# Kernel optimization log

Measured on AMD Instinct MI355X. Metric: run time of the kernel, lower is better.

Reference implementation:

```python
import jax, jax.numpy as jnp
import numpy as np

N_NODES = 50000
N_EDGES = 500000
IN_DIM = 128
H1, C1 = 4, 64   # layer1: heads=4, out=64, concat -> 256
H2, C2 = 1, 64   # layer2: heads=1, out=64


def setup_inputs() -> dict:
    key = jax.random.key(0)
    ks = jax.random.split(key, 16)
    p = lambda k, shp: (jax.random.normal(k, shp, dtype=jnp.float32) * 0.1)
    return {
        "x": jax.random.normal(ks[0], (N_NODES, IN_DIM), dtype=jnp.float32),
        "edge_index": jax.random.randint(ks[1], (2, N_EDGES), 0, N_NODES, dtype=jnp.int32),
        "edge_attr": jax.random.uniform(ks[2], (N_EDGES, 1), dtype=jnp.float32),
        # layer 1 params
        "W1": p(ks[3], (IN_DIM, H1 * C1)),
        "We1": p(ks[4], (1, H1 * C1)),
        "as1": p(ks[5], (H1, C1)),
        "ad1": p(ks[6], (H1, C1)),
        "ae1": p(ks[7], (H1, C1)),
        "b1": jnp.zeros((H1 * C1,), dtype=jnp.float32),
        # layer 2 params
        "W2": p(ks[8], (H1 * C1, H2 * C2)),
        "We2": p(ks[9], (1, H2 * C2)),
        "as2": p(ks[10], (H2, C2)),
        "ad2": p(ks[11], (H2, C2)),
        "ae2": p(ks[12], (H2, C2)),
        "b2": jnp.zeros((H2 * C2,), dtype=jnp.float32),
    }


def _add_self_loops(src, dst, edge_attr, n):
    # PyG fill_value='mean': loop edge_attr = mean of incoming edge attrs per node
    cnt = jax.ops.segment_sum(jnp.ones((src.shape[0],), edge_attr.dtype), dst, num_segments=n)
    loop_attr = jax.ops.segment_sum(edge_attr, dst, num_segments=n) / jnp.maximum(cnt, 1.0)[:, None]
    idx = jnp.arange(n, dtype=src.dtype)
    return (jnp.concatenate([src, idx]), jnp.concatenate([dst, idx]),
            jnp.concatenate([edge_attr, loop_attr], axis=0))


def _gat_conv(x, src, dst, edge_attr, W, We, a_src, a_dst, a_edge, bias, heads, out_ch):
    n = x.shape[0]
    h = (x @ W).reshape(n, heads, out_ch)                      # [N,H,C]
    e = (edge_attr @ We).reshape(-1, heads, out_ch)            # [E,H,C]
    alpha = ((h * a_src).sum(-1)[src]                          # gather src score
             + (h * a_dst).sum(-1)[dst]                        # gather dst score
             + (e * a_edge).sum(-1))                           # [E,H]
    alpha = jax.nn.leaky_relu(alpha, 0.2)
    m = jax.ops.segment_max(alpha, dst, num_segments=n)        # per-target max
    alpha = jnp.exp(alpha - m[dst])
    denom = jax.ops.segment_sum(alpha, dst, num_segments=n)
    alpha = alpha / (denom[dst] + 1e-16)
    out = jax.ops.segment_sum(h[src] * alpha[..., None], dst, num_segments=n)
    return out.reshape(n, heads * out_ch) + bias


def reference(x, edge_index, edge_attr, W1, We1, as1, ad1, ae1, b1,
              W2, We2, as2, ad2, ae2, b2):
    src, dst = edge_index[0], edge_index[1]
    src, dst, ea = _add_self_loops(src, dst, edge_attr, x.shape[0])
    h = jax.nn.elu(_gat_conv(x, src, dst, ea, W1, We1, as1, ad1, ae1, b1, H1, C1))
    return _gat_conv(h, src, dst, ea, W2, We2, as2, ad2, ae2, b2, H2, C2)
```

## Files before the change

### kernel.cpp

```cpp
#include <hip/hip_runtime.h>
#include <math.h>

#define NN 50000
#define NE 500000
#define DIM 128
#define HC1 256
#define HC2 64
#define RSTR 64
#define CAPM 63
#define EPB 1024
#define NBUCKET ((NE + EPB - 1) / EPB)
#define GB ((NN + 63) / 64)

typedef __attribute__((ext_vector_type(8))) short short8;
typedef __attribute__((ext_vector_type(4))) float floatx4;


__device__ __forceinline__ unsigned short f2bf(float f) {
  unsigned int u = __float_as_uint(f);
  unsigned int r = (u + 0x7FFFu + ((u >> 16) & 1u)) >> 16;
  return (unsigned short)r;
}
__device__ __forceinline__ float bf2f(unsigned short s) {
  return __uint_as_float(((unsigned int)s) << 16);
}

__device__ __forceinline__ float waveReduce(float v) {
  v += __shfl_down(v, 32);
  v += __shfl_down(v, 16);
  v += __shfl_down(v, 8);
  v += __shfl_down(v, 4);
  v += __shfl_down(v, 2);
  v += __shfl_down(v, 1);
  return v;
}


__global__ __launch_bounds__(256) void k_prep(const float* __restrict__ W1,
                                              const float* __restrict__ W2,
                                              const float* __restrict__ We1,
                                              const float* __restrict__ ae1,
                                              const float* __restrict__ We2,
                                              const float* __restrict__ ae2,
                                              unsigned short* __restrict__ W1T,
                                              unsigned short* __restrict__ W2T,
                                              float* __restrict__ ce,
                                              unsigned int* __restrict__ ebuf) {
  int b = blockIdx.x, t = threadIdx.x;
  if (b < 128) {
    int idx = b * 256 + t;
    int n = idx >> 7, k = idx & 127;
    W1T[idx] = f2bf(W1[k * 256 + n]);
  } else if (b < 192) {
    int idx = (b - 128) * 256 + t;
    int n = idx >> 8, k = idx & 255;
    W2T[idx] = f2bf(W2[k * 64 + n]);
  } else if (b == 192) {
    int h = t >> 6, lane = t & 63;
    float p = We1[h * 64 + lane] * ae1[h * 64 + lane];
    p = waveReduce(p);
    if (lane == 0) ce[h] = p;
    if (h == 0) {
      float q = We2[lane] * ae2[lane];
      q = waveReduce(q);
      if (lane == 0) ce[4] = q;
    }
  } else {
    int idx = (b - 193) * 256 + t;
    if (idx < NN) ebuf[(unsigned long long)idx * RSTR] = 0u;
  }
}


__global__ __launch_bounds__(256) void k_fused(const int* __restrict__ src,
                                               const int* __restrict__ dst,
                                               const float* __restrict__ ea,
                                               unsigned int* __restrict__ ebuf,
                                               const float* __restrict__ x,
                                               const unsigned short* __restrict__ W1T,
                                               const float* __restrict__ as1,
                                               const float* __restrict__ ad1,
                                               unsigned short* __restrict__ h1b,
                                               float* __restrict__ ss1,
                                               float* __restrict__ sd1) {
  __shared__ unsigned short As[64 * 136];
  int t = threadIdx.x;

  if (blockIdx.x < NBUCKET) {
    int e0 = blockIdx.x * EPB + t;
    int dv[4]; float ev[4]; unsigned int sv[4]; bool ok[4];
#pragma unroll
    for (int k = 0; k < 4; k++) {
      int e = e0 + k * 256;
      ok[k] = (e < NE);
      int ee = ok[k] ? e : 0;
      dv[k] = dst[ee];
      ev[k] = ea[ee];
      sv[k] = (unsigned int)src[ee];
    }
    unsigned int old[4];
#pragma unroll
    for (int k = 0; k < 4; k++) {
      if (ok[k]) old[k] = atomicAdd(&ebuf[(unsigned long long)dv[k] * RSTR], 1u);
    }
#pragma unroll
    for (int k = 0; k < 4; k++) {
      if (ok[k] && old[k] < CAPM) {
        unsigned int ea16 = __float2uint_rn(ev[k] * 65536.0f);
        if (ea16 > 65535u) ea16 = 65535u;
        ebuf[(unsigned long long)dv[k] * RSTR + 1 + old[k]] = (ea16 << 16) | sv[k];
      }
    }
    return;
  }

  int wave = t >> 6, lane = t & 63;
  int q = lane >> 4, ln = lane & 15;
  int m0 = (blockIdx.x - NBUCKET) * 64;
  int n0 = wave * 64;

  short8 bfr[4][4];
#pragma unroll
  for (int c = 0; c < 4; c++)
#pragma unroll
    for (int ks = 0; ks < 4; ks++)
      bfr[c][ks] = *(const short8*)&W1T[(n0 + ln * 4 + c) * 128 + ks * 32 + q * 8];

#pragma unroll
  for (int rep = 0; rep < 8; rep++) {
    int chunk = t + 256 * rep;
    int m = chunk >> 5, kk = (chunk & 31) * 4;
    int gr = m0 + m;
    float4 v = (gr < NN) ? *(const float4*)&x[gr * DIM + kk]
                         : make_float4(0.f, 0.f, 0.f, 0.f);
    ushort4 o;
    o.x = f2bf(v.x); o.y = f2bf(v.y); o.z = f2bf(v.z); o.w = f2bf(v.w);
    *(ushort4*)&As[m * 136 + kk] = o;
  }
  __syncthreads();

  floatx4 acc[4][4];
#pragma unroll
  for (int r = 0; r < 4; r++)
#pragma unroll
    for (int c = 0; c < 4; c++) acc[r][c] = (floatx4){0.f, 0.f, 0.f, 0.f};

#pragma unroll
  for (int ks = 0; ks < 4; ks++) {
    short8 afr[4];
#pragma unroll
    for (int r = 0; r < 4; r++)
      afr[r] = *(const short8*)&As[(r * 16 + ln) * 136 + ks * 32 + q * 8];
#pragma unroll
    for (int r = 0; r < 4; r++)
#pragma unroll
      for (int c = 0; c < 4; c++)
        acc[r][c] = __builtin_amdgcn_mfma_f32_16x16x32_bf16(afr[r], bfr[c][ks], acc[r][c], 0, 0, 0);
  }

  float4 a4 = *(const float4*)&as1[n0 + ln * 4];
  float4 d4 = *(const float4*)&ad1[n0 + ln * 4];

#pragma unroll
  for (int r = 0; r < 4; r++) {
#pragma unroll
    for (int i = 0; i < 4; i++) {
      int gm = m0 + r * 16 + q * 4 + i;
      if (gm < NN) {
        ushort4 o;
        o.x = f2bf(acc[r][0][i]);
        o.y = f2bf(acc[r][1][i]);
        o.z = f2bf(acc[r][2][i]);
        o.w = f2bf(acc[r][3][i]);
        *(ushort4*)&h1b[gm * HC1 + n0 + ln * 4] = o;
      }
      float ps = acc[r][0][i] * a4.x;
      float pd = acc[r][0][i] * d4.x;
      ps = fmaf(acc[r][1][i], a4.y, ps);
      pd = fmaf(acc[r][1][i], d4.y, pd);
      ps = fmaf(acc[r][2][i], a4.z, ps);
      pd = fmaf(acc[r][2][i], d4.z, pd);
      ps = fmaf(acc[r][3][i], a4.w, ps);
      pd = fmaf(acc[r][3][i], d4.w, pd);
#pragma unroll
      for (int m = 1; m < 16; m <<= 1) {
        ps += __shfl_xor(ps, m);
        pd += __shfl_xor(pd, m);
      }
      if (ln == 0 && gm < NN) {
        ss1[gm * 4 + wave] = ps;
        sd1[gm * 4 + wave] = pd;
      }
    }
  }
}


__global__ __launch_bounds__(1024) void k_agg1g2(const unsigned short* __restrict__ h1b,
                                                 const unsigned int* __restrict__ ebuf,
                                                 const float* __restrict__ ss1,
                                                 const float* __restrict__ sd1,
                                                 const float* __restrict__ ce,
                                                 const float* __restrict__ b1,
                                                 const unsigned short* __restrict__ W2T,
                                                 const float* __restrict__ as2,
                                                 const float* __restrict__ ad2,
                                                 unsigned short* __restrict__ h2b,
                                                 float* __restrict__ ss2,
                                                 float* __restrict__ sd2) {
  __shared__ unsigned short Ao[64 * 264];
  __shared__ float ssp[4][64], sdp[4][64];
  int t = threadIdx.x;
  int wave = t >> 6, lane = t & 63;
  int m0 = blockIdx.x * 64;

  {
    int h = lane >> 4;
    int c4 = lane * 4;
    int l16 = lane & 15;
    float ceh = ce[h];
    float4 bv = *(const float4*)&b1[c4];

    for (int nd = 0; nd < 4; nd++) {
      int vu = m0 + wave * 4 + nd;
      int lrow = wave * 4 + nd;
      if (vu >= NN) {
        ushort4 z = {0, 0, 0, 0};
        *(ushort4*)&Ao[lrow * 264 + c4] = z;
        continue;
      }
      unsigned int craw = ebuf[(unsigned long long)vu * RSTR];
      int cn = (craw < CAPM) ? (int)craw : CAPM;
      cn = __builtin_amdgcn_readfirstlane(cn);
      int beg1 = vu * RSTR + 1;
      int end1 = beg1 + cn;
      float sdh = sd1[vu * 4 + h];
      float4 acc = make_float4(0.f, 0.f, 0.f, 0.f);
      float l = 0.f;
      float easum = 0.f;

      for (int base = beg1; base < end1; base += 16) {
        unsigned int meta = ebuf[base + l16];
#pragma unroll
        for (int b4 = 0; b4 < 4; b4++) {
          if (base + b4 * 4 >= end1) break;
          float ssv[4], ea4[4];
          ushort4 u[4];
          bool vld[4];
#pragma unroll
          for (int jj = 0; jj < 4; jj++) {
            int j = b4 * 4 + jj;
            bool val = (base + j < end1);
            unsigned int m = __builtin_amdgcn_readlane(meta, j);
            int sj = val ? (int)(m & 0xFFFFu) : 0;
            ea4[jj] = (float)(m >> 16) * (1.0f / 65536.0f);
            vld[jj] = val;
            ssv[jj] = ss1[sj * 4 + h];
            u[jj] = *(const ushort4*)&h1b[sj * HC1 + c4];
          }
#pragma unroll
          for (int jj = 0; jj < 4; jj++) {
            easum += vld[jj] ? ea4[jj] : 0.f;
            float xx = fmaf(ea4[jj], ceh, ssv[jj] + sdh);
            xx = fmaxf(xx, 0.2f * xx);
            float a = vld[jj] ? __expf(xx) : 0.f;
            l += a;
            acc.x = fmaf(a, bf2f(u[jj].x), acc.x);
            acc.y = fmaf(a, bf2f(u[jj].y), acc.y);
            acc.z = fmaf(a, bf2f(u[jj].z), acc.z);
            acc.w = fmaf(a, bf2f(u[jj].w), acc.w);
          }
        }
      }
      {
        float lea = easum / fmaxf((float)cn, 1.0f);
        float xx = fmaf(lea, ceh, ss1[vu * 4 + h] + sdh);
        xx = fmaxf(xx, 0.2f * xx);
        float a = __expf(xx);
        ushort4 u = *(const ushort4*)&h1b[vu * HC1 + c4];
        l += a;
        acc.x = fmaf(a, bf2f(u.x), acc.x);
        acc.y = fmaf(a, bf2f(u.y), acc.y);
        acc.z = fmaf(a, bf2f(u.z), acc.z);
        acc.w = fmaf(a, bf2f(u.w), acc.w);
      }
      float inv = 1.f / (l + 1e-16f);
      float4 o;
      o.x = acc.x * inv + bv.x;
      o.y = acc.y * inv + bv.y;
      o.z = acc.z * inv + bv.z;
      o.w = acc.w * inv + bv.w;
      o.x = (o.x > 0.f) ? o.x : expm1f(o.x);
      o.y = (o.y > 0.f) ? o.y : expm1f(o.y);
      o.z = (o.z > 0.f) ? o.z : expm1f(o.z);
      o.w = (o.w > 0.f) ? o.w : expm1f(o.w);
      ushort4 ob;
      ob.x = f2bf(o.x); ob.y = f2bf(o.y); ob.z = f2bf(o.z); ob.w = f2bf(o.w);
      *(ushort4*)&Ao[lrow * 264 + c4] = ob;
    }
  }
  __syncthreads();

  {
    int q = lane >> 4, ln = lane & 15;
    int r = wave >> 2, c = wave & 3;

    short8 bfr[8];
#pragma unroll
    for (int ks = 0; ks < 8; ks++)
      bfr[ks] = *(const short8*)&W2T[(c * 16 + ln) * 256 + ks * 32 + q * 8];

    floatx4 acc = (floatx4){0.f, 0.f, 0.f, 0.f};
#pragma unroll
    for (int ks = 0; ks < 8; ks++) {
      short8 afr = *(const short8*)&Ao[(r * 16 + ln) * 264 + ks * 32 + q * 8];
      acc = __builtin_amdgcn_mfma_f32_16x16x32_bf16(afr, bfr[ks], acc, 0, 0, 0);
    }

    float as2v = as2[c * 16 + ln], ad2v = ad2[c * 16 + ln];
#pragma unroll
    for (int i = 0; i < 4; i++) {
      int gm = m0 + r * 16 + q * 4 + i;
      if (gm < NN) h2b[gm * HC2 + c * 16 + ln] = f2bf(acc[i]);
      float ps = acc[i] * as2v;
      float pd = acc[i] * ad2v;
#pragma unroll
      for (int m = 1; m < 16; m <<= 1) {
        ps += __shfl_xor(ps, m);
        pd += __shfl_xor(pd, m);
      }
      if (ln == 0) {
        ssp[c][r * 16 + q * 4 + i] = ps;
        sdp[c][r * 16 + q * 4 + i] = pd;
      }
    }
  }
  __syncthreads();
  if (t < 64) {
    int gm = m0 + t;
    if (gm < NN) {
      ss2[gm] = ssp[0][t] + ssp[1][t] + ssp[2][t] + ssp[3][t];
      sd2[gm] = sdp[0][t] + sdp[1][t] + sdp[2][t] + sdp[3][t];
    }
  }
}

__global__ __launch_bounds__(256) void k_agg2(const unsigned short* __restrict__ h2b,
                                              const unsigned int* __restrict__ ebuf,
                                              const float* __restrict__ ss2,
                                              const float* __restrict__ sd2,
                                              const float* __restrict__ ce,
                                              const float* __restrict__ b2,
                                              float* __restrict__ out) {
  int v = (blockIdx.x * blockDim.x + threadIdx.x) >> 6;
  int lane = threadIdx.x & 63;
  int g = lane >> 4;
  int c = lane & 15;
  int l16 = lane & 15;
  int vu = __builtin_amdgcn_readfirstlane(v);
  unsigned int craw = ebuf[(unsigned long long)vu * RSTR];
  int cn = (craw < CAPM) ? (int)craw : CAPM;
  cn = __builtin_amdgcn_readfirstlane(cn);
  int beg1 = vu * RSTR + 1;
  int end1 = beg1 + cn;
  float sdv = sd2[vu];
  float cev = ce[4];
  float4 acc = make_float4(0.f, 0.f, 0.f, 0.f);
  float l = 0.f;
  float easum = 0.f;

  for (int base = beg1; base < end1; base += 16) {
    int nb = end1 - base;
    unsigned int meta = ebuf[base + l16];
    float ssv[4], eav[4];
    bool vld[4];
    ushort4 u[4];
#pragma unroll
    for (int sub = 0; sub < 4; sub++) {
      int j = sub * 4 + g;
      bool val = (j < nb);
      unsigned int m = (unsigned int)__shfl((int)meta, j);
      int sj = val ? (int)(m & 0xFFFFu) : 0;
      eav[sub] = (float)(m >> 16) * (1.0f / 65536.0f);
      vld[sub] = val;
      ssv[sub] = ss2[sj];
      u[sub] = *(const ushort4*)&h2b[sj * HC2 + c * 4];
    }
#pragma unroll
    for (int sub = 0; sub < 4; sub++) {
      easum += vld[sub] ? eav[sub] : 0.f;
      float xx = fmaf(eav[sub], cev, ssv[sub] + sdv);
      xx = fmaxf(xx, 0.2f * xx);
      float a = vld[sub] ? __expf(xx) : 0.f;
      l += a;
      acc.x = fmaf(a, bf2f(u[sub].x), acc.x);
      acc.y = fmaf(a, bf2f(u[sub].y), acc.y);
      acc.z = fmaf(a, bf2f(u[sub].z), acc.z);
      acc.w = fmaf(a, bf2f(u[sub].w), acc.w);
    }
  }
#pragma unroll
  for (int m = 16; m <= 32; m <<= 1) {
    acc.x += __shfl_xor(acc.x, m);
    acc.y += __shfl_xor(acc.y, m);
    acc.z += __shfl_xor(acc.z, m);
    acc.w += __shfl_xor(acc.w, m);
    l += __shfl_xor(l, m);
    easum += __shfl_xor(easum, m);
  }
  {
    float lea = easum / fmaxf((float)cn, 1.0f);
    float xx = fmaf(lea, cev, ss2[vu] + sdv);
    xx = fmaxf(xx, 0.2f * xx);
    float a = __expf(xx);
    ushort4 us = *(const ushort4*)&h2b[vu * HC2 + c * 4];
    l += a;
    acc.x = fmaf(a, bf2f(us.x), acc.x);
    acc.y = fmaf(a, bf2f(us.y), acc.y);
    acc.z = fmaf(a, bf2f(us.z), acc.z);
    acc.w = fmaf(a, bf2f(us.w), acc.w);
  }
  if (g == 0) {
    float inv = 1.f / (l + 1e-16f);
    float4 bv = *(const float4*)&b2[c * 4];
    float4 o;
    o.x = acc.x * inv + bv.x;
    o.y = acc.y * inv + bv.y;
    o.z = acc.z * inv + bv.z;
    o.w = acc.w * inv + bv.w;
    *(float4*)&out[vu * HC2 + c * 4] = o;
  }
}


extern "C" void kernel_launch(void* const* d_in, const int* in_sizes, int n_in,
                              void* d_out, int out_size, void* d_ws, size_t ws_size,
                              hipStream_t stream) {
  const float* x   = (const float*)d_in[0];
  const int*   ei  = (const int*)d_in[1];
  const float* ea  = (const float*)d_in[2];
  const float* W1  = (const float*)d_in[3];
  const float* We1 = (const float*)d_in[4];
  const float* as1 = (const float*)d_in[5];
  const float* ad1 = (const float*)d_in[6];
  const float* ae1 = (const float*)d_in[7];
  const float* b1  = (const float*)d_in[8];
  const float* W2  = (const float*)d_in[9];
  const float* We2 = (const float*)d_in[10];
  const float* as2 = (const float*)d_in[11];
  const float* ad2 = (const float*)d_in[12];
  const float* ae2 = (const float*)d_in[13];
  const float* b2  = (const float*)d_in[14];
  const int* srcp = ei;
  const int* dstp = ei + NE;

  char* w = (char*)d_ws;
  float* ce      = (float*)(w + 0);
  float* ss1     = (float*)(w + 1024);
  float* sd1     = (float*)(w + 801024);
  float* ss2     = (float*)(w + 1601024);
  float* sd2     = (float*)(w + 1801024);
  unsigned int* ebuf = (unsigned int*)(w + 2001024);
  unsigned short* h1b = (unsigned short*)(w + 14801024);
  unsigned short* h2b = (unsigned short*)(w + 40401024);
  unsigned short* W1T = (unsigned short*)(w + 46801024);
  unsigned short* W2T = (unsigned short*)(w + 46866560);

  k_prep<<<389, 256, 0, stream>>>(W1, W2, We1, ae1, We2, ae2, W1T, W2T, ce, ebuf);
  k_fused<<<NBUCKET + GB, 256, 0, stream>>>(srcp, dstp, ea, ebuf,
                                            x, W1T, as1, ad1, h1b, ss1, sd1);

  k_agg1g2<<<GB, 1024, 0, stream>>>(h1b, ebuf, ss1, sd1, ce, b1,
                                    W2T, as2, ad2, h2b, ss2, sd2);

  k_agg2<<<(NN * 64 + 255) / 256, 256, 0, stream>>>(h2b, ebuf, ss2, sd2, ce, b2,
                                                    (float*)d_out);
}
```

Baseline: 229.4 us.

## Split edge counters into dense array, shrink agg1g2 blocks to four nodes

Moves the per-node edge counters out of the padded bucket rows into a dense, memset-cleared array, so atomics hit compact memory and each bucket row holds 64 edges. Edge bucketing now runs alongside the weight prep instead of sharing a launch with the first GEMM, and that GEMM gets its own kernel. The layer-1 aggregation plus layer-2 GEMM kernel now uses 256-thread blocks of four nodes with one node per wave, which raises block count and balance but wastes most of each 16-row MFMA tile. Layer-2 aggregation loads edge metadata per lane directly instead of using shuffles. The extra memset and kernel boundary add some launch overhead.

Measured after the change: 253.6 us. 1.11x slower.

```diff
diff --git a/kernel.cpp b/kernel.cpp
--- a/kernel.cpp
+++ b/kernel.cpp
@@ -7,7 +7,7 @@
 #define HC1 256
 #define HC2 64
 #define RSTR 64
-#define CAPM 63
+#define CAPM 64
 #define EPB 1024
 #define NBUCKET ((NE + EPB - 1) / EPB)
 #define GB ((NN + 63) / 64)
@@ -36,26 +36,58 @@
 }
 
 
-__global__ __launch_bounds__(256) void k_prep(const float* __restrict__ W1,
-                                              const float* __restrict__ W2,
-                                              const float* __restrict__ We1,
-                                              const float* __restrict__ ae1,
-                                              const float* __restrict__ We2,
-                                              const float* __restrict__ ae2,
-                                              unsigned short* __restrict__ W1T,
-                                              unsigned short* __restrict__ W2T,
-                                              float* __restrict__ ce,
-                                              unsigned int* __restrict__ ebuf) {
+__global__ __launch_bounds__(256) void k_bucketprep(const int* __restrict__ src,
+                                                    const int* __restrict__ dst,
+                                                    const float* __restrict__ ea,
+                                                    unsigned int* __restrict__ cnt,
+                                                    unsigned int* __restrict__ ebuf,
+                                                    const float* __restrict__ W1,
+                                                    const float* __restrict__ W2,
+                                                    const float* __restrict__ We1,
+                                                    const float* __restrict__ ae1,
+                                                    const float* __restrict__ We2,
+                                                    const float* __restrict__ ae2,
+                                                    unsigned short* __restrict__ W1T,
+                                                    unsigned short* __restrict__ W2T,
+                                                    float* __restrict__ ce) {
   int b = blockIdx.x, t = threadIdx.x;
-  if (b < 128) {
-    int idx = b * 256 + t;
+  if (b < NBUCKET) {
+    int e0 = b * EPB + t;
+    int dv[4]; float ev[4]; unsigned int sv[4]; bool ok[4];
+#pragma unroll
+    for (int k = 0; k < 4; k++) {
+      int e = e0 + k * 256;
+      ok[k] = (e < NE);
+      int ee = ok[k] ? e : 0;
+      dv[k] = dst[ee];
+      ev[k] = ea[ee];
+      sv[k] = (unsigned int)src[ee];
+    }
+    unsigned int old[4];
+#pragma unroll
+    for (int k = 0; k < 4; k++) {
+      if (ok[k]) old[k] = atomicAdd(&cnt[dv[k]], 1u);
+    }
+#pragma unroll
+    for (int k = 0; k < 4; k++) {
+      if (ok[k] && old[k] < CAPM) {
+        unsigned int ea16 = __float2uint_rn(ev[k] * 65536.0f);
+        if (ea16 > 65535u) ea16 = 65535u;
+        ebuf[(unsigned long long)dv[k] * RSTR + old[k]] = (ea16 << 16) | sv[k];
+      }
+    }
+    return;
+  }
+  int pb = b - NBUCKET;
+  if (pb < 128) {
+    int idx = pb * 256 + t;
     int n = idx >> 7, k = idx & 127;
     W1T[idx] = f2bf(W1[k * 256 + n]);
-  } else if (b < 192) {
-    int idx = (b - 128) * 256 + t;
+  } else if (pb < 192) {
+    int idx = (pb - 128) * 256 + t;
     int n = idx >> 8, k = idx & 255;
     W2T[idx] = f2bf(W2[k * 64 + n]);
-  } else if (b == 192) {
+  } else {
     int h = t >> 6, lane = t & 63;
     float p = We1[h * 64 + lane] * ae1[h * 64 + lane];
     p = waveReduce(p);
@@ -65,18 +97,11 @@
       q = waveReduce(q);
       if (lane == 0) ce[4] = q;
     }
-  } else {
-    int idx = (b - 193) * 256 + t;
-    if (idx < NN) ebuf[(unsigned long long)idx * RSTR] = 0u;
-  }
-}
-
-
-__global__ __launch_bounds__(256) void k_fused(const int* __restrict__ src,
-                                               const int* __restrict__ dst,
-                                               const float* __restrict__ ea,
-                                               unsigned int* __restrict__ ebuf,
-                                               const float* __restrict__ x,
+  }
+}
+
+
+__global__ __launch_bounds__(256) void k_gemm1(const float* __restrict__ x,
                                                const unsigned short* __restrict__ W1T,
                                                const float* __restrict__ as1,
                                                const float* __restrict__ ad1,
@@ -85,38 +110,9 @@
                                                float* __restrict__ sd1) {
   __shared__ unsigned short As[64 * 136];
   int t = threadIdx.x;
-
-  if (blockIdx.x < NBUCKET) {
-    int e0 = blockIdx.x * EPB + t;
-    int dv[4]; float ev[4]; unsigned int sv[4]; bool ok[4];
-#pragma unroll
-    for (int k = 0; k < 4; k++) {
-      int e = e0 + k * 256;
-      ok[k] = (e < NE);
-      int ee = ok[k] ? e : 0;
-      dv[k] = dst[ee];
-      ev[k] = ea[ee];
-      sv[k] = (unsigned int)src[ee];
-    }
-    unsigned int old[4];
-#pragma unroll
-    for (int k = 0; k < 4; k++) {
-      if (ok[k]) old[k] = atomicAdd(&ebuf[(unsigned long long)dv[k] * RSTR], 1u);
-    }
-#pragma unroll
-    for (int k = 0; k < 4; k++) {
-      if (ok[k] && old[k] < CAPM) {
-        unsigned int ea16 = __float2uint_rn(ev[k] * 65536.0f);
-        if (ea16 > 65535u) ea16 = 65535u;
-        ebuf[(unsigned long long)dv[k] * RSTR + 1 + old[k]] = (ea16 << 16) | sv[k];
-      }
-    }
-    return;
-  }
-
   int wave = t >> 6, lane = t & 63;
   int q = lane >> 4, ln = lane & 15;
-  int m0 = (blockIdx.x - NBUCKET) * 64;
+  int m0 = blockIdx.x * 64;
   int n0 = wave * 64;
 
   short8 bfr[4][4];
@@ -196,132 +192,130 @@
 }
 
 
-__global__ __launch_bounds__(1024) void k_agg1g2(const unsigned short* __restrict__ h1b,
-                                                 const unsigned int* __restrict__ ebuf,
-                                                 const float* __restrict__ ss1,
-                                                 const float* __restrict__ sd1,
-                                                 const float* __restrict__ ce,
-                                                 const float* __restrict__ b1,
-                                                 const unsigned short* __restrict__ W2T,
-                                                 const float* __restrict__ as2,
-                                                 const float* __restrict__ ad2,
-                                                 unsigned short* __restrict__ h2b,
-                                                 float* __restrict__ ss2,
-                                                 float* __restrict__ sd2) {
-  __shared__ unsigned short Ao[64 * 264];
-  __shared__ float ssp[4][64], sdp[4][64];
+__global__ __launch_bounds__(256) void k_agg1g2(const unsigned short* __restrict__ h1b,
+                                                const unsigned int* __restrict__ cnt,
+                                                const unsigned int* __restrict__ ebuf,
+                                                const float* __restrict__ ss1,
+                                                const float* __restrict__ sd1,
+                                                const float* __restrict__ ce,
+                                                const float* __restrict__ b1,
+                                                const unsigned short* __restrict__ W2T,
+                                                const float* __restrict__ as2,
+                                                const float* __restrict__ ad2,
+                                                unsigned short* __restrict__ h2b,
+                                                float* __restrict__ ss2,
+                                                float* __restrict__ sd2) {
+  __shared__ unsigned short Ao[16 * 264];
+  __shared__ float ssp[4][16], sdp[4][16];
   int t = threadIdx.x;
   int wave = t >> 6, lane = t & 63;
-  int m0 = blockIdx.x * 64;
+  int m0 = blockIdx.x * 4;
+  short8 zero8 = {0, 0, 0, 0, 0, 0, 0, 0};
+
+  for (int idx = t; idx < 12 * 32; idx += 256) {
+    int row = 4 + (idx >> 5), chunk = idx & 31;
+    *(short8*)&Ao[row * 264 + chunk * 8] = zero8;
+  }
 
   {
     int h = lane >> 4;
     int c4 = lane * 4;
     int l16 = lane & 15;
+    int vu = m0 + wave;
+    unsigned int craw = cnt[vu];
+    int cn = (craw < CAPM) ? (int)craw : CAPM;
+    cn = __builtin_amdgcn_readfirstlane(cn);
+    int beg1 = vu * RSTR;
+    int end1 = beg1 + cn;
+    float sdh = sd1[vu * 4 + h];
     float ceh = ce[h];
+    float4 acc = make_float4(0.f, 0.f, 0.f, 0.f);
+    float l = 0.f;
+    float easum = 0.f;
+
+    for (int base = beg1; base < end1; base += 16) {
+      unsigned int meta = ebuf[base + l16];
+#pragma unroll
+      for (int b4 = 0; b4 < 4; b4++) {
+        if (base + b4 * 4 >= end1) break;
+        float ssv[4], ea4[4];
+        ushort4 u[4];
+        bool vld[4];
+#pragma unroll
+        for (int jj = 0; jj < 4; jj++) {
+          int j = b4 * 4 + jj;
+          bool val = (base + j < end1);
+          unsigned int m = __builtin_amdgcn_readlane(meta, j);
+          int sj = val ? (int)(m & 0xFFFFu) : 0;
+          ea4[jj] = (float)(m >> 16) * (1.0f / 65536.0f);
+          vld[jj] = val;
+          ssv[jj] = ss1[sj * 4 + h];
+          u[jj] = *(const ushort4*)&h1b[sj * HC1 + c4];
+        }
+#pragma unroll
+        for (int jj = 0; jj < 4; jj++) {
+          easum += vld[jj] ? ea4[jj] : 0.f;
+          float xx = fmaf(ea4[jj], ceh, ssv[jj] + sdh);
+          xx = fmaxf(xx, 0.2f * xx);
+          float a = vld[jj] ? __expf(xx) : 0.f;
+          l += a;
+          acc.x = fmaf(a, bf2f(u[jj].x), acc.x);
+          acc.y = fmaf(a, bf2f(u[jj].y), acc.y);
+          acc.z = fmaf(a, bf2f(u[jj].z), acc.z);
+          acc.w = fmaf(a, bf2f(u[jj].w), acc.w);
+        }
+      }
+    }
+    {
+      float lea = easum / fmaxf((float)cn, 1.0f);
+      float xx = fmaf(lea, ceh, ss1[vu * 4 + h] + sdh);
+      xx = fmaxf(xx, 0.2f * xx);
+      float a = __expf(xx);
+      ushort4 u = *(const ushort4*)&h1b[vu * HC1 + c4];
+      l += a;
+      acc.x = fmaf(a, bf2f(u.x), acc.x);
+      acc.y = fmaf(a, bf2f(u.y), acc.y);
+      acc.z = fmaf(a, bf2f(u.z), acc.z);
+      acc.w = fmaf(a, bf2f(u.w), acc.w);
+    }
+    float inv = 1.f / (l + 1e-16f);
     float4 bv = *(const float4*)&b1[c4];
-
-    for (int nd = 0; nd < 4; nd++) {
-      int vu = m0 + wave * 4 + nd;
-      int lrow = wave * 4 + nd;
-      if (vu >= NN) {
-        ushort4 z = {0, 0, 0, 0};
-        *(ushort4*)&Ao[lrow * 264 + c4] = z;
-        continue;
-      }
-      unsigned int craw = ebuf[(unsigned long long)vu * RSTR];
-      int cn = (craw < CAPM) ? (int)craw : CAPM;
-      cn = __builtin_amdgcn_readfirstlane(cn);
-      int beg1 = vu * RSTR + 1;
-      int end1 = beg1 + cn;
-      float sdh = sd1[vu * 4 + h];
-      float4 acc = make_float4(0.f, 0.f, 0.f, 0.f);
-      float l = 0.f;
-      float easum = 0.f;
-
-      for (int base = beg1; base < end1; base += 16) {
-        unsigned int meta = ebuf[base + l16];
-#pragma unroll
-        for (int b4 = 0; b4 < 4; b4++) {
-          if (base + b4 * 4 >= end1) break;
-          float ssv[4], ea4[4];
-          ushort4 u[4];
-          bool vld[4];
-#pragma unroll
-          for (int jj = 0; jj < 4; jj++) {
-            int j = b4 * 4 + jj;
-            bool val = (base + j < end1);
-            unsigned int m = __builtin_amdgcn_readlane(meta, j);
-            int sj = val ? (int)(m & 0xFFFFu) : 0;
-            ea4[jj] = (float)(m >> 16) * (1.0f / 65536.0f);
-            vld[jj] = val;
-            ssv[jj] = ss1[sj * 4 + h];
-            u[jj] = *(const ushort4*)&h1b[sj * HC1 + c4];
-          }
-#pragma unroll
-          for (int jj = 0; jj < 4; jj++) {
-            easum += vld[jj] ? ea4[jj] : 0.f;
-            float xx = fmaf(ea4[jj], ceh, ssv[jj] + sdh);
-            xx = fmaxf(xx, 0.2f * xx);
-            float a = vld[jj] ? __expf(xx) : 0.f;
-            l += a;
-            acc.x = fmaf(a, bf2f(u[jj].x), acc.x);
-            acc.y = fmaf(a, bf2f(u[jj].y), acc.y);
-            acc.z = fmaf(a, bf2f(u[jj].z), acc.z);
-            acc.w = fmaf(a, bf2f(u[jj].w), acc.w);
-          }
-        }
-      }
-      {
-        float lea = easum / fmaxf((float)cn, 1.0f);
-        float xx = fmaf(lea, ceh, ss1[vu * 4 + h] + sdh);
-        xx = fmaxf(xx, 0.2f * xx);
-        float a = __expf(xx);
-        ushort4 u = *(const ushort4*)&h1b[vu * HC1 + c4];
-        l += a;
-        acc.x = fmaf(a, bf2f(u.x), acc.x);
-        acc.y = fmaf(a, bf2f(u.y), acc.y);
-        acc.z = fmaf(a, bf2f(u.z), acc.z);
-        acc.w = fmaf(a, bf2f(u.w), acc.w);
-      }
-      float inv = 1.f / (l + 1e-16f);
-      float4 o;
-      o.x = acc.x * inv + bv.x;
-      o.y = acc.y * inv + bv.y;
-      o.z = acc.z * inv + bv.z;
-      o.w = acc.w * inv + bv.w;
-      o.x = (o.x > 0.f) ? o.x : expm1f(o.x);
-      o.y = (o.y > 0.f) ? o.y : expm1f(o.y);
-      o.z = (o.z > 0.f) ? o.z : expm1f(o.z);
-      o.w = (o.w > 0.f) ? o.w : expm1f(o.w);
-      ushort4 ob;
-      ob.x = f2bf(o.x); ob.y = f2bf(o.y); ob.z = f2bf(o.z); ob.w = f2bf(o.w);
-      *(ushort4*)&Ao[lrow * 264 + c4] = ob;
-    }
+    float4 o;
+    o.x = acc.x * inv + bv.x;
+    o.y = acc.y * inv + bv.y;
+    o.z = acc.z * inv + bv.z;
+    o.w = acc.w * inv + bv.w;
+    o.x = (o.x > 0.f) ? o.x : expm1f(o.x);
+    o.y = (o.y > 0.f) ? o.y : expm1f(o.y);
+    o.z = (o.z > 0.f) ? o.z : expm1f(o.z);
+    o.w = (o.w > 0.f) ? o.w : expm1f(o.w);
+    ushort4 ob;
+    ob.x = f2bf(o.x); ob.y = f2bf(o.y); ob.z = f2bf(o.z); ob.w = f2bf(o.w);
+    *(ushort4*)&Ao[wave * 264 + c4] = ob;
   }
   __syncthreads();
 
   {
     int q = lane >> 4, ln = lane & 15;
-    int r = wave >> 2, c = wave & 3;
+    int c0 = wave * 16;
 
     short8 bfr[8];
 #pragma unroll
     for (int ks = 0; ks < 8; ks++)
-      bfr[ks] = *(const short8*)&W2T[(c * 16 + ln) * 256 + ks * 32 + q * 8];
+      bfr[ks] = *(const short8*)&W2T[(c0 + ln) * 256 + ks * 32 + q * 8];
 
     floatx4 acc = (floatx4){0.f, 0.f, 0.f, 0.f};
 #pragma unroll
     for (int ks = 0; ks < 8; ks++) {
-      short8 afr = *(const short8*)&Ao[(r * 16 + ln) * 264 + ks * 32 + q * 8];
+      short8 afr = *(const short8*)&Ao[ln * 264 + ks * 32 + q * 8];
       acc = __builtin_amdgcn_mfma_f32_16x16x32_bf16(afr, bfr[ks], acc, 0, 0, 0);
     }
 
-    float as2v = as2[c * 16 + ln], ad2v = ad2[c * 16 + ln];
+    float as2v = as2[c0 + ln], ad2v = ad2[c0 + ln];
 #pragma unroll
     for (int i = 0; i < 4; i++) {
-      int gm = m0 + r * 16 + q * 4 + i;
-      if (gm < NN) h2b[gm * HC2 + c * 16 + ln] = f2bf(acc[i]);
+      int row = q * 4 + i;
+      if (row < 4) h2b[(m0 + row) * HC2 + c0 + ln] = f2bf(acc[i]);
       float ps = acc[i] * as2v;
       float pd = acc[i] * ad2v;
 #pragma unroll
@@ -330,22 +324,21 @@
         pd += __shfl_xor(pd, m);
       }
       if (ln == 0) {
-        ssp[c][r * 16 + q * 4 + i] = ps;
-        sdp[c][r * 16 + q * 4 + i] = pd;
+        ssp[wave][row] = ps;
+        sdp[wave][row] = pd;
       }
     }
   }
   __syncthreads();
-  if (t < 64) {
-    int gm = m0 + t;
-    if (gm < NN) {
-      ss2[gm] = ssp[0][t] + ssp[1][t] + ssp[2][t] + ssp[3][t];
-      sd2[gm] = sdp[0][t] + sdp[1][t] + sdp[2][t] + sdp[3][t];
-    }
-  }
-}
+  if (t < 4) {
+    ss2[m0 + t] = ssp[0][t] + ssp[1][t] + ssp[2][t] + ssp[3][t];
+    sd2[m0 + t] = sdp[0][t] + sdp[1][t] + sdp[2][t] + sdp[3][t];
+  }
+}
+
 
 __global__ __launch_bounds__(256) void k_agg2(const unsigned short* __restrict__ h2b,
+                                              const unsigned int* __restrict__ cnt,
                                               const unsigned int* __restrict__ ebuf,
                                               const float* __restrict__ ss2,
                                               const float* __restrict__ sd2,
@@ -356,22 +349,19 @@
   int lane = threadIdx.x & 63;
   int g = lane >> 4;
   int c = lane & 15;
-  int l16 = lane & 15;
   int vu = __builtin_amdgcn_readfirstlane(v);
-  unsigned int craw = ebuf[(unsigned long long)vu * RSTR];
+  unsigned int craw = cnt[vu];
   int cn = (craw < CAPM) ? (int)craw : CAPM;
   cn = __builtin_amdgcn_readfirstlane(cn);
-  int beg1 = vu * RSTR + 1;
-  int end1 = beg1 + cn;
+  int beg1 = vu * RSTR;
   float sdv = sd2[vu];
   float cev = ce[4];
   float4 acc = make_float4(0.f, 0.f, 0.f, 0.f);
   float l = 0.f;
   float easum = 0.f;
 
-  for (int base = beg1; base < end1; base += 16) {
-    int nb = end1 - base;
-    unsigned int meta = ebuf[base + l16];
+  for (int j0 = 0; j0 < cn; j0 += 16) {
+    int nb = cn - j0;
     float ssv[4], eav[4];
     bool vld[4];
     ushort4 u[4];
@@ -379,7 +369,7 @@
     for (int sub = 0; sub < 4; sub++) {
       int j = sub * 4 + g;
       bool val = (j < nb);
-      unsigned int m = (unsigned int)__shfl((int)meta, j);
+      unsigned int m = ebuf[beg1 + j0 + (val ? j : 0)];
       int sj = val ? (int)(m & 0xFFFFu) : 0;
       eav[sub] = (float)(m >> 16) * (1.0f / 65536.0f);
       vld[sub] = val;
@@ -455,24 +445,28 @@
   const int* dstp = ei + NE;
 
   char* w = (char*)d_ws;
-  float* ce      = (float*)(w + 0);
-  float* ss1     = (float*)(w + 1024);
-  float* sd1     = (float*)(w + 801024);
-  float* ss2     = (float*)(w + 1601024);
-  float* sd2     = (float*)(w + 1801024);
-  unsigned int* ebuf = (unsigned int*)(w + 2001024);
-  unsigned short* h1b = (unsigned short*)(w + 14801024);
-  unsigned short* h2b = (unsigned short*)(w + 40401024);
-  unsigned short* W1T = (unsigned short*)(w + 46801024);
-  unsigned short* W2T = (unsigned short*)(w + 46866560);
-
-  k_prep<<<389, 256, 0, stream>>>(W1, W2, We1, ae1, We2, ae2, W1T, W2T, ce, ebuf);
-  k_fused<<<NBUCKET + GB, 256, 0, stream>>>(srcp, dstp, ea, ebuf,
-                                            x, W1T, as1, ad1, h1b, ss1, sd1);
-
-  k_agg1g2<<<GB, 1024, 0, stream>>>(h1b, ebuf, ss1, sd1, ce, b1,
-                                    W2T, as2, ad2, h2b, ss2, sd2);
-
-  k_agg2<<<(NN * 64 + 255) / 256, 256, 0, stream>>>(h2b, ebuf, ss2, sd2, ce, b2,
+  unsigned int* cnt = (unsigned int*)(w + 0);
+  float* ce      = (float*)(w + 200704);
+  float* ss1     = (float*)(w + 201728);
+  float* sd1     = (float*)(w + 1001728);
+  float* ss2     = (float*)(w + 1801728);
+  float* sd2     = (float*)(w + 2001728);
+  unsigned int* ebuf = (unsigned int*)(w + 2201728);
+  unsigned short* h1b = (unsigned short*)(w + 15001728);
+  unsigned short* h2b = (unsigned short*)(w + 40601728);
+  unsigned short* W1T = (unsigned short*)(w + 47001728);
+  unsigned short* W2T = (unsigned short*)(w + 47067264);
+
+  hipMemsetAsync(cnt, 0, 200000, stream);
+
+  k_bucketprep<<<NBUCKET + 193, 256, 0, stream>>>(srcp, dstp, ea, cnt, ebuf,
+                                                  W1, W2, We1, ae1, We2, ae2,
+                                                  W1T, W2T, ce);
+  k_gemm1<<<GB, 256, 0, stream>>>(x, W1T, as1, ad1, h1b, ss1, sd1);
+
+  k_agg1g2<<<(NN + 3) / 4, 256, 0, stream>>>(h1b, cnt, ebuf, ss1, sd1, ce, b1,
+                                             W2T, as2, ad2, h2b, ss2, sd2);
+
+  k_agg2<<<(NN * 64 + 255) / 256, 256, 0, stream>>>(h2b, cnt, ebuf, ss2, sd2, ce, b2,
                                                     (float*)d_out);
 }
```
